# Optimization experiments

Hardware: AMD Instinct MI355X
Metric: run time of the kernel (lower is better)

Reference implementation:

```python
import jax, jax.numpy as jnp
import numpy as np

N_EMBD = 1024
N_HEAD = 16
HEAD_SIZE = N_EMBD // N_HEAD  # 64
B, T = 4, 2048

def setup_inputs() -> dict:
    key = jax.random.key(0)
    k1, k2, k3, k4 = jax.random.split(key, 4)
    x = jax.random.normal(k1, (B, T, N_EMBD), dtype=jnp.float32)
    # weights stored as [in, out]; torch Linear does x @ W.T with W [out,in]
    w_qkv = jax.random.normal(k2, (N_EMBD, 3 * N_EMBD), dtype=jnp.float32) * (N_EMBD ** -0.5)
    w_proj = jax.random.normal(k3, (N_EMBD, N_EMBD), dtype=jnp.float32) * (N_EMBD ** -0.5)
    b_proj = jax.random.normal(k4, (N_EMBD,), dtype=jnp.float32) * 0.01
    return {"x": x, "w_qkv": w_qkv, "w_proj": w_proj, "b_proj": b_proj}

def reference(x, w_qkv, w_proj, b_proj):
    Bx, Tx, C = x.shape
    H, D = N_HEAD, HEAD_SIZE
    qkv = x @ w_qkv                               # [B,T,3C]
    q, k, v = jnp.split(qkv, 3, axis=-1)
    q = q.reshape(Bx, Tx, H, D).transpose(0, 2, 1, 3)  # [B,H,T,D]
    k = k.reshape(Bx, Tx, H, D).transpose(0, 2, 1, 3)
    v = v.reshape(Bx, Tx, H, D).transpose(0, 2, 1, 3)
    att = jnp.einsum('bhqd,bhkd->bhqk', q, k) * (D ** -0.5)  # [B,H,T,T]
    causal = jnp.tril(jnp.ones((Tx, Tx), dtype=bool))
    att = jnp.where(causal[None, None], att, -jnp.inf)
    att = jax.nn.softmax(att, axis=-1)
    out = jnp.einsum('bhqk,bhkd->bhqd', att, v)   # [B,H,T,D]
    out = out.transpose(0, 2, 1, 3).reshape(Bx, Tx, H * D)
    return out @ w_proj + b_proj
```

## Files before the change

kernel.cpp:

```cpp
#include <hip/hip_runtime.h>
#include <hip/hip_bf16.h>
#include <stdint.h>
#include <math.h>


typedef __attribute__((ext_vector_type(8))) short short8;
typedef __attribute__((ext_vector_type(4))) float f32x4;

#define LOG2E 1.44269504088896340736f
#define QSCALE 0.18033688011112042f

__device__ int g_isf32;

__device__ __forceinline__ void gl16(const void* g, void* l) {
  __builtin_amdgcn_global_load_lds(
      (const __attribute__((address_space(1))) unsigned int*)g,
      (__attribute__((address_space(3))) unsigned int*)l, 16, 0, 0);
}

__device__ __forceinline__ short f2bf(float f) {
  __hip_bfloat16 h = __float2bfloat16(f);
  return *reinterpret_cast<short*>(&h);
}
__device__ __forceinline__ float bf2f(short s) {
  __hip_bfloat16 h = *reinterpret_cast<__hip_bfloat16*>(&s);
  return __bfloat162float(h);
}
__device__ __forceinline__ short8 pack8(f32x4 lo, f32x4 hi) {
  short8 r;
#pragma unroll
  for (int e = 0; e < 4; ++e) { r[e] = f2bf(lo[e]); r[4 + e] = f2bf(hi[e]); }
  return r;
}

__device__ __forceinline__ unsigned cvtpk(float a, float b) {
  unsigned r;
  asm("v_cvt_pk_bf16_f32 %0, %1, %2" : "=v"(r) : "v"(a), "v"(b));
  return r;
}

__device__ __forceinline__ float dpp_sum16(float x) {
  int i;
  i = __builtin_amdgcn_update_dpp(0, __builtin_bit_cast(int, x), 0xB1, 0xF, 0xF, true);
  x += __builtin_bit_cast(float, i);
  i = __builtin_amdgcn_update_dpp(0, __builtin_bit_cast(int, x), 0x4E, 0xF, 0xF, true);
  x += __builtin_bit_cast(float, i);
  i = __builtin_amdgcn_update_dpp(0, __builtin_bit_cast(int, x), 0x141, 0xF, 0xF, true);
  x += __builtin_bit_cast(float, i);
  i = __builtin_amdgcn_update_dpp(0, __builtin_bit_cast(int, x), 0x140, 0xF, 0xF, true);
  x += __builtin_bit_cast(float, i);
  return x;
}

__global__ __launch_bounds__(256) void detect_dtype(const unsigned short* w) {
  __shared__ int cnt;
  if (threadIdx.x == 0) cnt = 0;
  __syncthreads();
  const unsigned short* p = w + (long)blockIdx.x * 49152;
  int c = 0;
  for (int i = threadIdx.x; i < 49152; i += 256)
    if (((p[i] >> 7) & 0xFF) == 0xFF) c++;
  atomicAdd(&cnt, c);
  __syncthreads();
  if (threadIdx.x == 0) g_isf32 = (cnt > 8) ? 1 : 0;
}

__global__ __launch_bounds__(256) void cvt_x(const void* __restrict__ src,
                                             short* __restrict__ dst) {
  const long i = ((long)blockIdx.x * 256 + threadIdx.x) * 8;
  if (g_isf32) {
    const float* s = (const float*)src + i;
    *(short8*)(dst + i) = pack8(*(const f32x4*)s, *(const f32x4*)(s + 4));
  } else {
    *(short8*)(dst + i) = *(const short8*)((const short*)src + i);
  }
}

template <int MODE>
__global__ __launch_bounds__(512, 2) void gemm_bt(
    const short* __restrict__ A, const short* __restrict__ Bt,
    const void* __restrict__ bias, void* __restrict__ C,
    short* __restrict__ vt, int M, int N, int K)
{
  __shared__ __align__(16) short As[3][16384];
  __shared__ __align__(16) short Bs[3][8192];
  const int tid  = threadIdx.x;
  const int lane = tid & 63;
  const int wave = tid >> 6;
  const int quad = lane >> 4;
  const int l16  = lane & 15;
  const int wm = (wave >> 1) * 64;
  const int wn = (wave & 1) * 64;

  const int gx = (int)gridDim.x;
  const int nwg = gx * (int)gridDim.y;
  int lb = (int)blockIdx.y * gx + (int)blockIdx.x;
  if ((nwg & 7) == 0) lb = (lb & 7) * (nwg >> 3) + (lb >> 3);
  const long m0 = (long)(lb / gx) * 256;
  const long n0 = (long)(lb % gx) * 128;

  int isf32 = 0;
  if (MODE == 1) {
    isf32 = g_isf32;
    asm volatile("s_waitcnt vmcnt(0) lgkmcnt(0)" ::: "memory");
  }

  f32x4 acc[4][4] = {};

  const int srow = tid >> 3;
  const int scol = ((tid & 7) ^ (srow & 7)) * 8;
  const short* Ag = A  + (m0 + srow) * (long)K + scol;
  const short* Bg = Bt + (n0 + srow) * (long)K + scol;
  const long rs64 = (long)64 * K;

  const int x7  = l16 & 7;
  const int xo0 = ((0 + quad) ^ x7) * 16;
  const int xo1 = ((4 + quad) ^ x7) * 16;
  const int aRow = (wm + l16) * 128;
  const int bRow = (wn + l16) * 128;

  auto STAGE_HALF = [&](int t2, int h) {
    const int bb = t2 % 3;
    const long k0 = (long)t2 << 6;
    gl16(Ag + k0 + (h * 2 + 0) * rs64, (char*)As[bb] + (h * 2 + 0) * 8192 + tid * 16);
    gl16(Ag + k0 + (h * 2 + 1) * rs64, (char*)As[bb] + (h * 2 + 1) * 8192 + tid * 16);
    gl16(Bg + k0 + h * rs64,           (char*)Bs[bb] + h * 8192 + tid * 16);
  };

  const int nt = K >> 6;
  STAGE_HALF(0, 0); STAGE_HALF(0, 1);
  STAGE_HALF(1, 0); STAGE_HALF(1, 1);

  for (int t = 0; t < nt; ++t) {
    if (t + 1 < nt) { asm volatile("s_waitcnt vmcnt(6)" ::: "memory"); }
    else            { asm volatile("s_waitcnt vmcnt(0)" ::: "memory"); }
    __builtin_amdgcn_sched_barrier(0);
    __builtin_amdgcn_s_barrier();
    __builtin_amdgcn_sched_barrier(0);

    const char* Ab = (const char*)As[t % 3];
    const char* Bb = (const char*)Bs[t % 3];

#pragma unroll
    for (int ph = 0; ph < 2; ++ph) {
      const int xo = ph ? xo1 : xo0;
      short8 af[4], bfv[4];
#pragma unroll
      for (int i = 0; i < 4; ++i)
        af[i] = *(const short8*)(Ab + aRow + i * 2048 + xo);
#pragma unroll
      for (int j = 0; j < 4; ++j)
        bfv[j] = *(const short8*)(Bb + bRow + j * 2048 + xo);
      if (t + 2 < nt) STAGE_HALF(t + 2, ph);
      __builtin_amdgcn_s_setprio(1);
#pragma unroll
      for (int i = 0; i < 4; ++i)
#pragma unroll
        for (int j = 0; j < 4; ++j)
          acc[i][j] = __builtin_amdgcn_mfma_f32_16x16x32_bf16(af[i], bfv[j], acc[i][j], 0, 0, 0);
      __builtin_amdgcn_s_setprio(0);
      if (ph == 0) {
        __builtin_amdgcn_s_barrier();
        __builtin_amdgcn_sched_barrier(0);
      }
    }
  }

#pragma unroll
  for (int j = 0; j < 4; ++j) {
    const long col = n0 + wn + j * 16 + l16;
    if (MODE == 2 && col >= 2048) {
      const long hd = col - 2048;
      const long bb = (m0 + wm) >> 11;
      const long tb = (m0 + wm) & 2047;
      short* vrow = vt + ((bb * 16 + (hd >> 6)) * 64 + (hd & 63)) * 2048 + tb;
#pragma unroll
      for (int ip = 0; ip < 2; ++ip)
#pragma unroll
        for (int r = 0; r < 4; ++r)
          *(unsigned*)&vrow[ip * 32 + 2 * (quad * 4 + r)] =
              cvtpk(acc[2 * ip][j][r], acc[2 * ip + 1][j][r]);
    } else {
      float bv = 0.f;
      if (MODE == 1)
        bv = isf32 ? ((const float*)bias)[col] : bf2f(((const short*)bias)[col]);
#pragma unroll
      for (int i = 0; i < 4; ++i) {
        const long row0 = m0 + wm + i * 16 + quad * 4;
#pragma unroll
        for (int r = 0; r < 4; ++r) {
          const long row = row0 + r;
          const float val = acc[i][j][r] + bv;
          if (MODE == 2) {
            const float vq = (col < 1024) ? val * QSCALE : val;
            ((short*)C)[row * 2048 + col] = f2bf(vq);
          } else {
            if (isf32) ((float*)C)[row * (long)N + col] = val;
            else       ((short*)C)[row * (long)N + col] = f2bf(val);
          }
        }
      }
    }
  }
}

__global__ __launch_bounds__(256) void transpose64(
    const void* __restrict__ src, short* __restrict__ dst, int R, int C)
{
  __shared__ __align__(16) short tile[64][72];
  const int isf32 = g_isf32;
  const int tid = threadIdx.x;
  const long r0 = (long)blockIdx.y * 64;
  const long c0 = (long)blockIdx.x * 64;
#pragma unroll
  for (int it = 0; it < 2; ++it) {
    int idx = it * 256 + tid;
    int rr = idx >> 3, ch = idx & 7;
    const long off = (r0 + rr) * C + c0 + ch * 8;
    short8 v;
    if (isf32) {
      const float* s = (const float*)src + off;
      v = pack8(*(const f32x4*)s, *(const f32x4*)(s + 4));
    } else {
      v = *(const short8*)((const short*)src + off);
    }
    *(short8*)&tile[rr][ch * 8] = v;
  }
  __syncthreads();
#pragma unroll
  for (int it = 0; it < 2; ++it) {
    int idx = it * 256 + tid;
    int cc = idx >> 3, ch = idx & 7;
    short8 v;
#pragma unroll
    for (int jj = 0; jj < 8; ++jj) v[jj] = tile[ch * 8 + jj][cc];
    *(short8*)&dst[(c0 + cc) * R + r0 + ch * 8] = v;
  }
}

__global__ __launch_bounds__(512) void attn_fwd(
    const short* __restrict__ qk, const short* __restrict__ vt,
    short* __restrict__ out)
{
  __shared__ __align__(16) short Ks[2][2][64][32];
  __shared__ __align__(16) short Vs[2][2][64][32];
  __shared__ __align__(16) unsigned Pw[8][16][40];
  const int tid = threadIdx.x;
  const int lane = tid & 63, wave = tid >> 6;
  const int quad = lane >> 4, l16 = lane & 15;
  const int bh = blockIdx.x;
  const int b = bh >> 4, h = bh & 15;

  const int shalf = tid >> 8;
  const int srow  = (tid >> 2) & 63;
  const int sc    = (tid & 3) ^ (srow & 3);
  const short* kg = qk + (long)b * 2048 * 2048 + 1024 + h * 64
                      + (long)srow * 2048 + shalf * 32 + sc * 8;
  const short* vg = vt + ((long)bh * 64 + srow) * 2048 + shalf * 32 + sc * 8;

  const int fx = (quad ^ (l16 & 3)) * 16;

  const int s = 15 - (int)blockIdx.y;
  const int nt = 2 * s + 2;
  const int qb = s * 128 + wave * 16;
  const int qlast = qb + 15;

  const short* qp = qk + ((long)(b * 2048 + qb + l16)) * 2048 + h * 64 + quad * 8;
  const short8 aq0 = *(const short8*)qp;
  const short8 aq1 = *(const short8*)(qp + 32);

  gl16(kg,                    (char*)Ks[0] + tid * 16);
  gl16(vg,                    (char*)Vs[0] + tid * 16);
  gl16(kg + (long)64 * 2048,  (char*)Ks[1] + tid * 16);
  gl16(vg + 64,               (char*)Vs[1] + tid * 16);

  f32x4 o[4] = {};
  float l_run[4] = {0.f, 0.f, 0.f, 0.f};

  for (int kt = 0; kt < nt; ++kt) {
    if (kt + 1 < nt) { asm volatile("s_waitcnt vmcnt(2)" ::: "memory"); }
    else             { asm volatile("s_waitcnt vmcnt(0)" ::: "memory"); }
    __builtin_amdgcn_sched_barrier(0);
    __builtin_amdgcn_s_barrier();
    __builtin_amdgcn_sched_barrier(0);

    const int k0 = kt * 64;
    const int rb0 = kt & 1;
    if (k0 <= qlast) {
      const bool full = (k0 + 63 <= qb);
      const bool h2 = (k0 + 32 <= qlast);

      float p[4][4];
#pragma unroll
      for (int c = 0; c < 4; ++c) {
        if (full || (k0 + c * 16 <= qlast)) {
          short8 kf0 = *(const short8*)((const char*)&Ks[rb0][0][c * 16 + l16][0] + fx);
          short8 kf1 = *(const short8*)((const char*)&Ks[rb0][1][c * 16 + l16][0] + fx);
          f32x4 z = {};
          z = __builtin_amdgcn_mfma_f32_16x16x32_bf16(aq0, kf0, z, 0, 0, 0);
          z = __builtin_amdgcn_mfma_f32_16x16x32_bf16(aq1, kf1, z, 0, 0, 0);
          if (!full) {
#pragma unroll
            for (int r = 0; r < 4; ++r)
              z[r] = (k0 + c * 16 + l16 > qb + quad * 4 + r) ? -1e30f : z[r];
          }
#pragma unroll
          for (int r = 0; r < 4; ++r) {
            p[c][r] = __builtin_amdgcn_exp2f(z[r]);
            l_run[r] += p[c][r];
          }
        } else {
#pragma unroll
          for (int r = 0; r < 4; ++r) p[c][r] = 0.f;
        }
      }
#pragma unroll
      for (int r = 0; r < 4; ++r) {
        Pw[wave][quad * 4 + r][l16] = cvtpk(p[0][r], p[1][r]);
        if (h2) Pw[wave][quad * 4 + r][16 + l16] = cvtpk(p[2][r], p[3][r]);
      }

      {
        short8 pf0 = *(const short8*)&Pw[wave][l16][quad * 4];
#pragma unroll
        for (int i = 0; i < 4; ++i) {
          short8 vf0 = *(const short8*)((const char*)&Vs[rb0][0][i * 16 + l16][0] + fx);
          o[i] = __builtin_amdgcn_mfma_f32_16x16x32_bf16(pf0, vf0, o[i], 0, 0, 0);
        }
        if (h2) {
          short8 pf1 = *(const short8*)&Pw[wave][l16][16 + quad * 4];
#pragma unroll
          for (int i = 0; i < 4; ++i) {
            short8 vf1 = *(const short8*)((const char*)&Vs[rb0][1][i * 16 + l16][0] + fx);
            o[i] = __builtin_amdgcn_mfma_f32_16x16x32_bf16(pf1, vf1, o[i], 0, 0, 0);
          }
        }
      }
    }

    __builtin_amdgcn_s_barrier();
    __builtin_amdgcn_sched_barrier(0);
    if (kt + 2 < nt) {
      gl16(kg + (long)((kt + 2) * 64) * 2048, (char*)Ks[rb0] + tid * 16);
      gl16(vg + (kt + 2) * 64,                (char*)Vs[rb0] + tid * 16);
    }
  }

#pragma unroll
  for (int r = 0; r < 4; ++r) l_run[r] = dpp_sum16(l_run[r]);
  float inv[4];
#pragma unroll
  for (int r = 0; r < 4; ++r) inv[r] = 1.0f / l_run[r];
  short* op = out + ((long)(b * 2048 + qb + quad * 4)) * 1024 + h * 64;
#pragma unroll
  for (int i = 0; i < 4; ++i)
#pragma unroll
    for (int r = 0; r < 4; ++r)
      op[(long)r * 1024 + i * 16 + l16] = f2bf(o[i][r] * inv[r]);
}

__global__ __launch_bounds__(256) void copy_out(const void* __restrict__ src,
                                                void* __restrict__ dst)
{
  const long n16 = g_isf32 ? 2097152L : 1048576L;
  const uint4* s = (const uint4*)src;
  uint4* d = (uint4*)dst;
  for (long i = (long)blockIdx.x * 256 + threadIdx.x; i < n16;
       i += (long)gridDim.x * 256)
    d[i] = s[i];
}

extern "C" void kernel_launch(void* const* d_in, const int* in_sizes, int n_in,
                              void* d_out, int out_size, void* d_ws, size_t ws_size,
                              hipStream_t stream)
{
  const void* x      = d_in[0];
  const void* w_qkv  = d_in[1];
  const void* w_proj = d_in[2];
  const void* b_proj = d_in[3];

  short* ws = (short*)d_ws;
  const bool planA = ws_size >= 67108864ULL;

  short* qk  = ws;
  short* vtp = ws + 16777216L;

  short *wqkvT, *attnb, *wprojT, *xbf;
  void*  projC;
  if (planA) {
    attnb  = ws + 25165824L;
    wqkvT  = attnb;
    wprojT = qk;
    xbf    = (short*)d_out;
    projC  = d_out;
  } else {
    wqkvT  = (short*)d_out;
    xbf    = (short*)d_out + 3145728L;
    attnb  = (short*)d_out;
    wprojT = vtp;
    projC  = qk;
  }

  detect_dtype<<<64, 256, 0, stream>>>((const unsigned short*)w_qkv);
  cvt_x<<<4096, 256, 0, stream>>>(x, xbf);
  transpose64<<<dim3(3072 / 64, 1024 / 64), 256, 0, stream>>>(w_qkv, wqkvT, 1024, 3072);
  gemm_bt<2><<<dim3(3072 / 128, 8192 / 256), 512, 0, stream>>>(
      xbf, wqkvT, nullptr, qk, vtp, 8192, 3072, 1024);
  attn_fwd<<<dim3(64, 16), 512, 0, stream>>>(qk, vtp, attnb);
  transpose64<<<dim3(1024 / 64, 1024 / 64), 256, 0, stream>>>(w_proj, wprojT, 1024, 1024);
  gemm_bt<1><<<dim3(1024 / 128, 8192 / 256), 512, 0, stream>>>(
      attnb, wprojT, b_proj, projC, nullptr, 8192, 1024, 1024);
  if (!planA)
    copy_out<<<2048, 256, 0, stream>>>(projC, d_out);
}
```

Before: 270.9 us.

## Fuse x conversion with w_qkv transpose and split attention P staging in halves

Merges the x fp32-to-bf16 conversion and the w_qkv transpose into one prep kernel with a block-index split, which saves a launch and lets both jobs run in the same grid. In the attention kernel, the per-wave P scratch shrinks from 40 to 16 columns. Scores for the second 32-key half are now computed only after the first half's PV MMA, reusing the same LDS region. That lowers register and LDS pressure, but it serializes the two halves through the same buffer with an extra write/read round-trip.

```diff
diff --git a/kernel.cpp b/kernel.cpp
--- a/kernel.cpp
+++ b/kernel.cpp
@@ -65,14 +65,52 @@
   if (threadIdx.x == 0) g_isf32 = (cnt > 8) ? 1 : 0;
 }
 
-__global__ __launch_bounds__(256) void cvt_x(const void* __restrict__ src,
-                                             short* __restrict__ dst) {
-  const long i = ((long)blockIdx.x * 256 + threadIdx.x) * 8;
-  if (g_isf32) {
-    const float* s = (const float*)src + i;
-    *(short8*)(dst + i) = pack8(*(const f32x4*)s, *(const f32x4*)(s + 4));
+__global__ __launch_bounds__(256) void prep(const void* __restrict__ x,
+                                            short* __restrict__ xbf,
+                                            const void* __restrict__ wqkv,
+                                            short* __restrict__ wqkvT)
+{
+  __shared__ __align__(16) short tile[64][72];
+  const int isf32 = g_isf32;
+  const int bid = (int)blockIdx.x;
+  const int tid = threadIdx.x;
+  if (bid < 4096) {
+    const long i = ((long)bid * 256 + tid) * 8;
+    if (isf32) {
+      const float* s = (const float*)x + i;
+      *(short8*)(xbf + i) = pack8(*(const f32x4*)s, *(const f32x4*)(s + 4));
+    } else {
+      *(short8*)(xbf + i) = *(const short8*)((const short*)x + i);
+    }
   } else {
-    *(short8*)(dst + i) = *(const short8*)((const short*)src + i);
+    const int tb = bid - 4096;
+    const long c0 = (long)(tb % 48) * 64;
+    const long r0 = (long)(tb / 48) * 64;
+    const int C = 3072, R = 1024;
+#pragma unroll
+    for (int it = 0; it < 2; ++it) {
+      int idx = it * 256 + tid;
+      int rr = idx >> 3, ch = idx & 7;
+      const long off = (r0 + rr) * C + c0 + ch * 8;
+      short8 v;
+      if (isf32) {
+        const float* s = (const float*)wqkv + off;
+        v = pack8(*(const f32x4*)s, *(const f32x4*)(s + 4));
+      } else {
+        v = *(const short8*)((const short*)wqkv + off);
+      }
+      *(short8*)&tile[rr][ch * 8] = v;
+    }
+    __syncthreads();
+#pragma unroll
+    for (int it = 0; it < 2; ++it) {
+      int idx = it * 256 + tid;
+      int cc = idx >> 3, ch = idx & 7;
+      short8 v;
+#pragma unroll
+      for (int jj = 0; jj < 8; ++jj) v[jj] = tile[ch * 8 + jj][cc];
+      *(short8*)&wqkvT[(c0 + cc) * R + r0 + ch * 8] = v;
+    }
   }
 }
 
@@ -244,7 +282,7 @@
 {
   __shared__ __align__(16) short Ks[2][2][64][32];
   __shared__ __align__(16) short Vs[2][2][64][32];
-  __shared__ __align__(16) unsigned Pw[8][16][40];
+  __shared__ __align__(16) unsigned Pw[8][16][16];
   const int tid = threadIdx.x;
   const int lane = tid & 63, wave = tid >> 6;
   const int quad = lane >> 4, l16 = lane & 15;
@@ -290,9 +328,9 @@
       const bool full = (k0 + 63 <= qb);
       const bool h2 = (k0 + 32 <= qlast);
 
-      float p[4][4];
-#pragma unroll
-      for (int c = 0; c < 4; ++c) {
+      float p[2][4];
+#pragma unroll
+      for (int c = 0; c < 2; ++c) {
         if (full || (k0 + c * 16 <= qlast)) {
           short8 kf0 = *(const short8*)((const char*)&Ks[rb0][0][c * 16 + l16][0] + fx);
           short8 kf1 = *(const short8*)((const char*)&Ks[rb0][1][c * 16 + l16][0] + fx);
@@ -315,11 +353,8 @@
         }
       }
 #pragma unroll
-      for (int r = 0; r < 4; ++r) {
+      for (int r = 0; r < 4; ++r)
         Pw[wave][quad * 4 + r][l16] = cvtpk(p[0][r], p[1][r]);
-        if (h2) Pw[wave][quad * 4 + r][16 + l16] = cvtpk(p[2][r], p[3][r]);
-      }
-
       {
         short8 pf0 = *(const short8*)&Pw[wave][l16][quad * 4];
 #pragma unroll
@@ -327,8 +362,38 @@
           short8 vf0 = *(const short8*)((const char*)&Vs[rb0][0][i * 16 + l16][0] + fx);
           o[i] = __builtin_amdgcn_mfma_f32_16x16x32_bf16(pf0, vf0, o[i], 0, 0, 0);
         }
-        if (h2) {
-          short8 pf1 = *(const short8*)&Pw[wave][l16][16 + quad * 4];
+      }
+
+      if (h2) {
+#pragma unroll
+        for (int c = 0; c < 2; ++c) {
+          const int cc = c + 2;
+          if (full || (k0 + cc * 16 <= qlast)) {
+            short8 kf0 = *(const short8*)((const char*)&Ks[rb0][0][cc * 16 + l16][0] + fx);
+            short8 kf1 = *(const short8*)((const char*)&Ks[rb0][1][cc * 16 + l16][0] + fx);
+            f32x4 z = {};
+            z = __builtin_amdgcn_mfma_f32_16x16x32_bf16(aq0, kf0, z, 0, 0, 0);
+            z = __builtin_amdgcn_mfma_f32_16x16x32_bf16(aq1, kf1, z, 0, 0, 0);
+            if (!full) {
+#pragma unroll
+              for (int r = 0; r < 4; ++r)
+                z[r] = (k0 + cc * 16 + l16 > qb + quad * 4 + r) ? -1e30f : z[r];
+            }
+#pragma unroll
+            for (int r = 0; r < 4; ++r) {
+              p[c][r] = __builtin_amdgcn_exp2f(z[r]);
+              l_run[r] += p[c][r];
+            }
+          } else {
+#pragma unroll
+            for (int r = 0; r < 4; ++r) p[c][r] = 0.f;
+          }
+        }
+#pragma unroll
+        for (int r = 0; r < 4; ++r)
+          Pw[wave][quad * 4 + r][l16] = cvtpk(p[0][r], p[1][r]);
+        {
+          short8 pf1 = *(const short8*)&Pw[wave][l16][quad * 4];
 #pragma unroll
           for (int i = 0; i < 4; ++i) {
             short8 vf1 = *(const short8*)((const char*)&Vs[rb0][1][i * 16 + l16][0] + fx);
@@ -402,8 +467,7 @@
   }
 
   detect_dtype<<<64, 256, 0, stream>>>((const unsigned short*)w_qkv);
-  cvt_x<<<4096, 256, 0, stream>>>(x, xbf);
-  transpose64<<<dim3(3072 / 64, 1024 / 64), 256, 0, stream>>>(w_qkv, wqkvT, 1024, 3072);
+  prep<<<4864, 256, 0, stream>>>(x, xbf, w_qkv, wqkvT);
   gemm_bt<2><<<dim3(3072 / 128, 8192 / 256), 512, 0, stream>>>(
       xbf, wqkvT, nullptr, qk, vtp, 8192, 3072, 1024);
   attn_fwd<<<dim3(64, 16), 512, 0, stream>>>(qk, vtp, attnb);
```

Result: slower. 278.3 us (+2.7%).
